# Optimization experiments

Measured on AMD Instinct MI355X. Metric: run time of the kernel, lower is better.

The kernel has to match this reference:

```python
import jax, jax.numpy as jnp
import numpy as np

NHEAD = 8
LAYER_NAMES = ('self', 'cross', 'self', 'cross')
EPS = 1e-6


def ln(x, g, b, eps=1e-5):
    m = jnp.mean(x, -1, keepdims=True)
    v = jnp.mean((x - m) ** 2, -1, keepdims=True)
    return (x - m) * jax.lax.rsqrt(v + eps) * g + b


def linear_attention(q, k, v, q_mask, kv_mask):
    # q: [N, L, H, D], k/v: [N, S, H, D]; LoFTR LinearAttention (elu+1 feature map)
    Q = jax.nn.elu(q) + 1.0
    K = jax.nn.elu(k) + 1.0
    if q_mask is not None:
        Q = Q * q_mask[:, :, None, None].astype(Q.dtype)
    if kv_mask is not None:
        mk = kv_mask[:, :, None, None].astype(K.dtype)
        K = K * mk
        v = v * mk
    v_len = v.shape[1]
    v = v / v_len
    KV = jnp.einsum('nshd,nshv->nhdv', K, v)
    Z = 1.0 / (jnp.einsum('nlhd,nhd->nlh', Q, K.sum(1)) + EPS)
    return jnp.einsum('nlhd,nhdv,nlh->nlhv', Q, KV, Z) * v_len


def enc_layer(x, src, q_mask, kv_mask, Wq, Wk, Wv, Wm, W1, W2, g1, b1, g2, b2):
    # x: [N, L, C], src: [N, S, C]
    N, L, C = x.shape
    S = src.shape[1]
    H, D = NHEAD, C // NHEAD
    q = (x @ Wq).reshape(N, L, H, D)
    k = (src @ Wk).reshape(N, S, H, D)
    v = (src @ Wv).reshape(N, S, H, D)
    msg = linear_attention(q, k, v, q_mask, kv_mask).reshape(N, L, C)
    msg = ln(msg @ Wm, g1, b1)
    msg = ln(jnp.tanh(jnp.concatenate([x, msg], axis=-1) @ W1) @ W2, g2, b2)
    return x + msg


def sample_descriptors(kp, fmap, s):
    # kp: [B, L, K, 2] (x, y) raw-image pixel coords; fmap: [B, C, H, W]; s: stride
    B, C, H, W = fmap.shape
    k = kp - s / 2 + 0.5
    denom = jnp.array([W * s - s / 2 - 0.5, H * s - s / 2 - 0.5], dtype=kp.dtype)
    k = (k / denom) * 2.0 - 1.0  # normalized [-1, 1]
    px = (k[..., 0] + 1.0) * 0.5 * (W - 1)  # align_corners=True grid_sample
    py = (k[..., 1] + 1.0) * 0.5 * (H - 1)
    x0 = jnp.floor(px)
    y0 = jnp.floor(py)
    wx = (px - x0)[..., None]
    wy = (py - y0)[..., None]
    x0i = jnp.clip(x0, 0, W - 1).astype(jnp.int32)
    x1i = jnp.clip(x0 + 1, 0, W - 1).astype(jnp.int32)
    y0i = jnp.clip(y0, 0, H - 1).astype(jnp.int32)
    y1i = jnp.clip(y0 + 1, 0, H - 1).astype(jnp.int32)
    fm = jnp.transpose(fmap, (0, 2, 3, 1))  # [B, H, W, C]
    bidx = jnp.arange(B)[:, None, None]
    g00 = fm[bidx, y0i, x0i]
    g01 = fm[bidx, y0i, x1i]
    g10 = fm[bidx, y1i, x0i]
    g11 = fm[bidx, y1i, x1i]
    out = (1 - wy) * ((1 - wx) * g00 + wx * g01) + wy * ((1 - wx) * g10 + wx * g11)
    # SuperPoint-style L2 normalization of sampled descriptors
    out = out / (jnp.linalg.norm(out, axis=-1, keepdims=True) + 1e-8)
    return out  # [B, L, K, C]


def geo_transformer(feat0, feat1, kp0_cross, kp1_cross, mask_self0, mask_self1,
                    mask_cross0, mask_cross1, Wq, Wk, Wv, Wm, W1, W2, g1, b1, g2, b2,
                    h0, w0, h1, w1, scale):
    B, L0, C = feat0.shape
    L1 = feat1.shape[1]
    K = kp0_cross.shape[2]
    for i, name in enumerate(LAYER_NAMES):
        p = (Wq[i], Wk[i], Wv[i], Wm[i], W1[i], W2[i], g1[i], b1[i], g2[i], b2[i])
        if name == 'self':
            # source = masked subset of x == full source with kv-mask (v_length cancels)
            feat0 = enc_layer(feat0, feat0, None, mask_self0, *p)
            feat1 = enc_layer(feat1, feat1, None, mask_self1, *p)
        else:
            fmap0 = jnp.transpose(feat0.reshape(B, h0, w0, C), (0, 3, 1, 2))
            fmap1 = jnp.transpose(feat1.reshape(B, h1, w1, C), (0, 3, 1, 2))
            f0c = sample_descriptors(kp0_cross, fmap0, scale)  # [B, L1, K, C]
            f1c = sample_descriptors(kp1_cross, fmap1, scale)  # [B, L0, K, C]
            x0 = feat0.reshape(B * L0, 1, C)
            x1 = feat1.reshape(B * L1, 1, C)
            nf0 = enc_layer(x0, f1c.reshape(B * L0, K, C), None,
                            mask_cross1.reshape(B * L0, K), *p)
            nf1 = enc_layer(x1, f0c.reshape(B * L1, K, C), None,
                            mask_cross0.reshape(B * L1, K), *p)
            feat0 = nf0.reshape(B, L0, C)
            feat1 = nf1.reshape(B, L1, C)
    return feat0, feat1


def setup_inputs() -> dict:
    key = jax.random.key(0)
    B, H0, W0, C, K, S, NL = 2, 64, 64, 256, 9, 8, 4
    L = H0 * W0
    ks = jax.random.split(key, 16)
    std = (2.0 / (C + C)) ** 0.5
    std2 = (2.0 / (2 * C + 2 * C)) ** 0.5
    std3 = (2.0 / (2 * C + C)) ** 0.5
    kp0 = jnp.stack([
        jax.random.uniform(ks[2], (B, L, K)) * (W0 * S),
        jax.random.uniform(ks[3], (B, L, K)) * (H0 * S)], axis=-1)
    kp1 = jnp.stack([
        jax.random.uniform(ks[4], (B, L, K)) * (W0 * S),
        jax.random.uniform(ks[5], (B, L, K)) * (H0 * S)], axis=-1)
    return {
        'feat0': jax.random.normal(ks[0], (B, L, C), jnp.float32),
        'feat1': jax.random.normal(ks[1], (B, L, C), jnp.float32),
        'kp0_cross': kp0.astype(jnp.float32),
        'kp1_cross': kp1.astype(jnp.float32),
        'mask_self0': jax.random.bernoulli(ks[6], 0.9, (B, L)),
        'mask_self1': jax.random.bernoulli(ks[7], 0.9, (B, L)),
        'mask_cross0': jax.random.bernoulli(ks[8], 0.8, (B, L, K)),
        'mask_cross1': jax.random.bernoulli(ks[9], 0.8, (B, L, K)),
        'Wq': jax.random.normal(ks[10], (NL, C, C), jnp.float32) * std,
        'Wk': jax.random.normal(ks[11], (NL, C, C), jnp.float32) * std,
        'Wv': jax.random.normal(ks[12], (NL, C, C), jnp.float32) * std,
        'Wm': jax.random.normal(ks[13], (NL, C, C), jnp.float32) * std,
        'W1': jax.random.normal(ks[14], (NL, 2 * C, 2 * C), jnp.float32) * std2,
        'W2': jax.random.normal(ks[15], (NL, 2 * C, C), jnp.float32) * std3,
        'g1': jnp.ones((NL, C), jnp.float32),
        'b1': jnp.zeros((NL, C), jnp.float32),
        'g2': jnp.ones((NL, C), jnp.float32),
        'b2': jnp.zeros((NL, C), jnp.float32),
        'h0': H0, 'w0': W0, 'h1': H0, 'w1': W0, 'scale': S,
    }


def reference(feat0, feat1, kp0_cross, kp1_cross, mask_self0, mask_self1,
              mask_cross0, mask_cross1, Wq, Wk, Wv, Wm, W1, W2, g1, b1, g2, b2,
              h0, w0, h1, w1, scale):
    return geo_transformer(feat0, feat1, kp0_cross, kp1_cross, mask_self0, mask_self1,
                           mask_cross0, mask_cross1, Wq, Wk, Wv, Wm, W1, W2,
                           g1, b1, g2, b2, h0, w0, h1, w1, scale)
```

## Files before the change

kernel.cpp:

```cpp
#include <hip/hip_runtime.h>
#include <cstddef>


#define NROWS 16384

typedef unsigned short ushort_t;
typedef __attribute__((ext_vector_type(8))) short short8;
typedef __attribute__((ext_vector_type(4))) float f32x4;
typedef __attribute__((ext_vector_type(4))) unsigned short ushort4_t;
typedef __attribute__((ext_vector_type(8))) unsigned short ushort8_t;

__device__ __forceinline__ float b2f(unsigned short u) {
    union { unsigned int i; float f; } v; v.i = (unsigned int)u << 16; return v.f;
}
__device__ __forceinline__ unsigned short f2b(float x) {
    union { float f; unsigned int i; } v; v.f = x;
    unsigned int r = v.i + 0x7fffu + ((v.i >> 16) & 1u);
    return (unsigned short)(r >> 16);
}
__device__ __forceinline__ float elu1(float x) {
    return x > 0.f ? x + 1.f : __expf(x);
}

#define ASYNC_COPY16(gptr, lptr) \
    __builtin_amdgcn_global_load_lds((const __attribute__((address_space(1))) void*)(gptr), \
                                     (__attribute__((address_space(3))) void*)(lptr), 16, 0, 0)

__global__ __launch_bounds__(256) void gemm_bf16_kernel(
    const ushort_t* __restrict__ A0, int lda0,
    const ushort_t* __restrict__ Wt, int ldw,
    ushort_t* __restrict__ C, int ldc, int Kd)
{
    __shared__ ushort_t As[128 * 64];
    __shared__ ushort_t Bs[128 * 64];

    int tid = threadIdx.x;
    int m0 = blockIdx.y * 128;
    int n0 = blockIdx.x * 128;
    int lane = tid & 63, w = tid >> 6;
    int wrow = w >> 1, wcol = w & 1;
    int quad = lane >> 4, l16 = lane & 15;

    f32x4 acc[4][4];
    #pragma unroll
    for (int i = 0; i < 4; i++)
        #pragma unroll
        for (int j = 0; j < 4; j++) acc[i][j] = (f32x4){0.f, 0.f, 0.f, 0.f};

    for (int kb = 0; kb < Kd; kb += 64) {
        #pragma unroll
        for (int q = 0; q < 4; q++) {
            int s = q * 256 + tid;
            int kk = s >> 9, p = s & 511;
            int row = p >> 2, c4 = p & 3;
            ASYNC_COPY16(A0 + (size_t)(m0 + row) * lda0 + kb + kk * 32 + c4 * 8,
                         (char*)As + s * 16);
        }
        #pragma unroll
        for (int q = 0; q < 4; q++) {
            int s = q * 256 + tid;
            int kk = s >> 9, p = s & 511;
            int row = p >> 2, c4 = p & 3;
            ASYNC_COPY16(Wt + (size_t)(n0 + row) * ldw + kb + kk * 32 + c4 * 8,
                         (char*)Bs + s * 16);
        }
        __syncthreads();

        #pragma unroll
        for (int kk = 0; kk < 2; kk++) {
            short8 af[4], bf[4];
            #pragma unroll
            for (int mt = 0; mt < 4; mt++)
                af[mt] = *(const short8*)&As[kk * 4096 + (wrow * 64 + mt * 16 + l16) * 32 + quad * 8];
            #pragma unroll
            for (int nt = 0; nt < 4; nt++)
                bf[nt] = *(const short8*)&Bs[kk * 4096 + (wcol * 64 + nt * 16 + l16) * 32 + quad * 8];
            #pragma unroll
            for (int mt = 0; mt < 4; mt++)
                #pragma unroll
                for (int nt = 0; nt < 4; nt++)
                    acc[mt][nt] = __builtin_amdgcn_mfma_f32_16x16x32_bf16(
                        af[mt], bf[nt], acc[mt][nt], 0, 0, 0);
        }
        __syncthreads();
    }

    #pragma unroll
    for (int mt = 0; mt < 4; mt++) {
        int row = m0 + wrow * 64 + mt * 16 + quad * 4;
        #pragma unroll
        for (int nt = 0; nt < 4; nt++) {
            int col = n0 + wcol * 64 + nt * 16 + l16;
            #pragma unroll
            for (int r = 0; r < 4; r++)
                C[(size_t)(row + r) * ldc + col] = f2b(acc[mt][nt][r]);
        }
    }
}

__global__ __launch_bounds__(256) void gemm_ln_kernel(
    const ushort_t* __restrict__ A, int lda,
    const ushort_t* __restrict__ Wt, int ldw, int Kd,
    const float* __restrict__ g, const float* __restrict__ bp,
    ushort_t* __restrict__ OutBf)
{
    __shared__ ushort_t As[32 * 64];
    __shared__ ushort_t Bs[256 * 64];
    __shared__ float rsum[4][32];
    __shared__ float rsq[4][32];

    int tid = threadIdx.x;
    int m0 = blockIdx.x * 32;
    int lane = tid & 63, w = tid >> 6;
    int quad = lane >> 4, l16 = lane & 15;

    f32x4 acc[2][4];
    #pragma unroll
    for (int i = 0; i < 2; i++)
        #pragma unroll
        for (int j = 0; j < 4; j++) acc[i][j] = (f32x4){0.f, 0.f, 0.f, 0.f};

    for (int kb = 0; kb < Kd; kb += 64) {
        {
            int s = tid;
            int kk = s >> 7, p = s & 127;
            int row = p >> 2, c4 = p & 3;
            ASYNC_COPY16(A + (size_t)(m0 + row) * lda + kb + kk * 32 + c4 * 8,
                         (char*)As + s * 16);
        }
        #pragma unroll
        for (int q = 0; q < 8; q++) {
            int s = q * 256 + tid;
            int kk = s >> 10, p = s & 1023;
            int row = p >> 2, c4 = p & 3;
            ASYNC_COPY16(Wt + (size_t)(row) * ldw + kb + kk * 32 + c4 * 8,
                         (char*)Bs + s * 16);
        }
        __syncthreads();

        #pragma unroll
        for (int kk = 0; kk < 2; kk++) {
            short8 af[2], bf[4];
            #pragma unroll
            for (int mt = 0; mt < 2; mt++)
                af[mt] = *(const short8*)&As[kk * 1024 + (mt * 16 + l16) * 32 + quad * 8];
            #pragma unroll
            for (int nt = 0; nt < 4; nt++)
                bf[nt] = *(const short8*)&Bs[kk * 8192 + (w * 64 + nt * 16 + l16) * 32 + quad * 8];
            #pragma unroll
            for (int mt = 0; mt < 2; mt++)
                #pragma unroll
                for (int nt = 0; nt < 4; nt++)
                    acc[mt][nt] = __builtin_amdgcn_mfma_f32_16x16x32_bf16(
                        af[mt], bf[nt], acc[mt][nt], 0, 0, 0);
        }
        __syncthreads();
    }

    #pragma unroll
    for (int mt = 0; mt < 2; mt++)
        #pragma unroll
        for (int r = 0; r < 4; r++) {
            float s = 0.f, q = 0.f;
            #pragma unroll
            for (int nt = 0; nt < 4; nt++) {
                float v = acc[mt][nt][r];
                s += v; q += v * v;
            }
            #pragma unroll
            for (int off = 1; off < 16; off <<= 1) {
                s += __shfl_xor(s, off, 64);
                q += __shfl_xor(q, off, 64);
            }
            if (l16 == 0) {
                rsum[w][mt * 16 + quad * 4 + r] = s;
                rsq[w][mt * 16 + quad * 4 + r]  = q;
            }
        }
    __syncthreads();

    #pragma unroll
    for (int mt = 0; mt < 2; mt++) {
        #pragma unroll
        for (int r = 0; r < 4; r++) {
            int rl = mt * 16 + quad * 4 + r;
            float s = rsum[0][rl] + rsum[1][rl] + rsum[2][rl] + rsum[3][rl];
            float q = rsq[0][rl] + rsq[1][rl] + rsq[2][rl] + rsq[3][rl];
            float m = s * (1.f / 256.f);
            float var = q * (1.f / 256.f) - m * m;
            float rs = rsqrtf(var + 1e-5f);
            size_t row = (size_t)(m0 + rl);
            #pragma unroll
            for (int nt = 0; nt < 4; nt++) {
                int col = w * 64 + nt * 16 + l16;
                float y = (acc[mt][nt][r] - m) * rs * g[col] + bp[col];
                OutBf[row * 256 + col] = f2b(y);
            }
        }
    }
}

__global__ __launch_bounds__(256) void mlp_fused_kernel(
    const ushort_t* __restrict__ Xb, const ushort_t* __restrict__ L1,
    const ushort_t* __restrict__ W1t, const ushort_t* __restrict__ W2t,
    const float* __restrict__ g, const float* __restrict__ bp,
    ushort_t* __restrict__ XbfOut, const float* __restrict__ Xin,
    float* __restrict__ Xout)
{
    __shared__ ushort_t Tt[32 * 512];
    __shared__ char buf[20480];

    ushort_t* As  = (ushort_t*)buf;
    ushort_t* Bs  = (ushort_t*)(buf + 4096);
    ushort_t* Bs2 = (ushort_t*)buf;
    float* rsum = (float*)buf;
    float* rsq  = (float*)(buf + 512);

    int tid = threadIdx.x;
    int m0 = blockIdx.x * 32;
    int lane = tid & 63, w = tid >> 6;
    int quad = lane >> 4, l16 = lane & 15;

    for (int np = 0; np < 4; np++) {
        f32x4 acc[2][2];
        #pragma unroll
        for (int i = 0; i < 2; i++)
            #pragma unroll
            for (int j = 0; j < 2; j++) acc[i][j] = (f32x4){0.f, 0.f, 0.f, 0.f};

        for (int kb = 0; kb < 512; kb += 64) {
            const ushort_t* Ab = (kb < 256) ? Xb : L1;
            int kc = (kb < 256) ? kb : kb - 256;
            {
                int s = tid;
                int kk = s >> 7, p = s & 127;
                ASYNC_COPY16(Ab + (size_t)(m0 + (p >> 2)) * 256 + kc + kk * 32 + (p & 3) * 8,
                             (char*)As + s * 16);
            }
            #pragma unroll
            for (int q = 0; q < 4; q++) {
                int s = q * 256 + tid;
                int kk = s >> 9, p = s & 511;
                ASYNC_COPY16(W1t + (size_t)(np * 128 + (p >> 2)) * 512 + kb + kk * 32 + (p & 3) * 8,
                             (char*)Bs + s * 16);
            }
            __syncthreads();

            #pragma unroll
            for (int kk = 0; kk < 2; kk++) {
                short8 af[2], bfr[2];
                #pragma unroll
                for (int mt = 0; mt < 2; mt++)
                    af[mt] = *(const short8*)&As[kk * 1024 + (mt * 16 + l16) * 32 + quad * 8];
                #pragma unroll
                for (int nt = 0; nt < 2; nt++)
                    bfr[nt] = *(const short8*)&Bs[kk * 4096 + (w * 32 + nt * 16 + l16) * 32 + quad * 8];
                #pragma unroll
                for (int mt = 0; mt < 2; mt++)
                    #pragma unroll
                    for (int nt = 0; nt < 2; nt++)
                        acc[mt][nt] = __builtin_amdgcn_mfma_f32_16x16x32_bf16(
                            af[mt], bfr[nt], acc[mt][nt], 0, 0, 0);
            }
            __syncthreads();
        }

        #pragma unroll
        for (int mt = 0; mt < 2; mt++)
            #pragma unroll
            for (int nt = 0; nt < 2; nt++)
                #pragma unroll
                for (int r = 0; r < 4; r++) {
                    int trow = mt * 16 + quad * 4 + r;
                    int col = np * 128 + w * 32 + nt * 16 + l16;
                    int c8s = (col >> 3) ^ (trow & 7);
                    Tt[trow * 512 + c8s * 8 + (col & 7)] = f2b(tanhf(acc[mt][nt][r]));
                }
    }

    f32x4 acc2[2][2][2];
    #pragma unroll
    for (int a = 0; a < 2; a++)
        #pragma unroll
        for (int i = 0; i < 2; i++)
            #pragma unroll
            for (int j = 0; j < 2; j++) acc2[a][i][j] = (f32x4){0.f, 0.f, 0.f, 0.f};

    for (int pass = 0; pass < 2; pass++) {
        for (int kb = 0; kb < 512; kb += 64) {
            #pragma unroll
            for (int q = 0; q < 4; q++) {
                int s = q * 256 + tid;
                int kk = s >> 9, p = s & 511;
                ASYNC_COPY16(W2t + (size_t)(pass * 128 + (p >> 2)) * 512 + kb + kk * 32 + (p & 3) * 8,
                             (char*)Bs2 + s * 16);
            }
            __syncthreads();

            #pragma unroll
            for (int kk = 0; kk < 2; kk++) {
                short8 af[2], bfr[2];
                #pragma unroll
                for (int mt = 0; mt < 2; mt++) {
                    int row = mt * 16 + l16;
                    int blk = ((kb >> 3) + kk * 4 + quad) ^ (row & 7);
                    af[mt] = *(const short8*)&Tt[row * 512 + blk * 8];
                }
                #pragma unroll
                for (int nt = 0; nt < 2; nt++)
                    bfr[nt] = *(const short8*)&Bs2[kk * 4096 + (w * 32 + nt * 16 + l16) * 32 + quad * 8];
                #pragma unroll
                for (int mt = 0; mt < 2; mt++)
                    #pragma unroll
                    for (int nt = 0; nt < 2; nt++)
                        acc2[pass][mt][nt] = __builtin_amdgcn_mfma_f32_16x16x32_bf16(
                            af[mt], bfr[nt], acc2[pass][mt][nt], 0, 0, 0);
            }
            __syncthreads();
        }
    }

    #pragma unroll
    for (int mt = 0; mt < 2; mt++)
        #pragma unroll
        for (int r = 0; r < 4; r++) {
            float s = 0.f, q = 0.f;
            #pragma unroll
            for (int pass = 0; pass < 2; pass++)
                #pragma unroll
                for (int nt = 0; nt < 2; nt++) {
                    float v = acc2[pass][mt][nt][r];
                    s += v; q += v * v;
                }
            #pragma unroll
            for (int off = 1; off < 16; off <<= 1) {
                s += __shfl_xor(s, off, 64);
                q += __shfl_xor(q, off, 64);
            }
            if (l16 == 0) {
                rsum[w * 32 + mt * 16 + quad * 4 + r] = s;
                rsq[w * 32 + mt * 16 + quad * 4 + r]  = q;
            }
        }
    __syncthreads();

    #pragma unroll
    for (int mt = 0; mt < 2; mt++) {
        #pragma unroll
        for (int r = 0; r < 4; r++) {
            int rl = mt * 16 + quad * 4 + r;
            float s = rsum[rl] + rsum[32 + rl] + rsum[64 + rl] + rsum[96 + rl];
            float q = rsq[rl] + rsq[32 + rl] + rsq[64 + rl] + rsq[96 + rl];
            float m = s * (1.f / 256.f);
            float var = q * (1.f / 256.f) - m * m;
            float rs = rsqrtf(var + 1e-5f);
            size_t row = (size_t)(m0 + rl);
            #pragma unroll
            for (int pass = 0; pass < 2; pass++)
                #pragma unroll
                for (int nt = 0; nt < 2; nt++) {
                    int col = pass * 128 + w * 32 + nt * 16 + l16;
                    float y = (acc2[pass][mt][nt][r] - m) * rs * g[col] + bp[col];
                    float xn = Xin[row * 256 + col] + y;
                    Xout[row * 256 + col] = xn;
                    XbfOut[row * 256 + col] = f2b(xn);
                }
        }
    }
}

__global__ __launch_bounds__(256) void wprep_kernel(
    const float* __restrict__ Wq, const float* __restrict__ Wk,
    const float* __restrict__ Wv, const float* __restrict__ Wm,
    const float* __restrict__ W1, const float* __restrict__ W2,
    ushort_t* __restrict__ Wqkvt, ushort_t* __restrict__ Wmt,
    ushort_t* __restrict__ W1t, ushort_t* __restrict__ W2t)
{
    int t = blockIdx.x;
    int layer = t / 640, r = t % 640;
    const float* src; ushort_t* dst;
    int ldsrc, lddst, tn, tk;
    if (r < 192) {
        int grp = r / 64, rr = r % 64; tn = rr / 8; tk = rr % 8;
        src = (grp == 0 ? Wq : grp == 1 ? Wk : Wv) + (size_t)layer * 65536;
        ldsrc = 256;
        dst = Wqkvt + (size_t)layer * 196608 + (size_t)grp * 65536;
        lddst = 256;
    } else if (r < 256) {
        int rr = r - 192; tn = rr / 8; tk = rr % 8;
        src = Wm + (size_t)layer * 65536; ldsrc = 256;
        dst = Wmt + (size_t)layer * 65536; lddst = 256;
    } else if (r < 512) {
        int rr = r - 256; tn = rr / 16; tk = rr % 16;
        src = W1 + (size_t)layer * 262144; ldsrc = 512;
        dst = W1t + (size_t)layer * 262144; lddst = 512;
    } else {
        int rr = r - 512; tn = rr / 16; tk = rr % 16;
        src = W2 + (size_t)layer * 131072; ldsrc = 256;
        dst = W2t + (size_t)layer * 131072; lddst = 512;
    }
    int n0 = tn * 32, k0 = tk * 32;
    __shared__ float tileS[32][33];
    int j = threadIdx.x & 31, i0 = threadIdx.x >> 5;
    #pragma unroll
    for (int p = 0; p < 4; p++) {
        int i = i0 + p * 8;
        tileS[i][j] = src[(size_t)(k0 + i) * ldsrc + n0 + j];
    }
    __syncthreads();
    #pragma unroll
    for (int p = 0; p < 4; p++) {
        int i = i0 + p * 8;
        dst[(size_t)(n0 + i) * lddst + k0 + j] = f2b(tileS[j][i]);
    }
}

__global__ __launch_bounds__(256) void init_kernel(
    const float* __restrict__ f0, const float* __restrict__ f1,
    float* __restrict__ X, ushort_t* __restrict__ Xbf)
{
    int idx = blockIdx.x * 256 + threadIdx.x;
    size_t e = (size_t)idx * 4;
    float4 v = (e < 2097152) ? *(const float4*)&f0[e] : *(const float4*)&f1[e - 2097152];
    *(float4*)&X[e] = v;
    ushort4_t u = { f2b(v.x), f2b(v.y), f2b(v.z), f2b(v.w) };
    *(ushort4_t*)&Xbf[e] = u;
}

__global__ __launch_bounds__(256) void kv_reduce_kernel(
    const ushort_t* __restrict__ QKV,
    const int* __restrict__ mask0, const int* __restrict__ mask1,
    float* __restrict__ KV, float* __restrict__ Ksum)
{
    int g = blockIdx.y;
    int t = g >> 4, b = (g >> 3) & 1, h = g & 7;
    const int* mask = t ? mask1 : mask0;
    int rowbase = t * 8192 + b * 4096;
    int s_begin = blockIdx.x * 256;

    __shared__ float sK[32][32];
    __shared__ float sV[32][32];

    int tid = threadIdx.x;
    int e  = tid & 31;
    int dq = tid >> 5;

    float acc[4] = {0.f, 0.f, 0.f, 0.f};
    float ks[4]  = {0.f, 0.f, 0.f, 0.f};

    for (int s0 = s_begin; s0 < s_begin + 256; s0 += 32) {
        #pragma unroll
        for (int q = 0; q < 2; q++) {
            int idx = tid + q * 256;
            int rl = idx >> 4;
            int part = idx & 15;
            int s = s0 + rl;
            size_t row = (size_t)(rowbase + s);
            float m = mask[b * 4096 + s] ? 1.f : 0.f;
            if (part < 8) {
                ushort4_t u = *(const ushort4_t*)&QKV[row * 768 + 256 + h * 32 + part * 4];
                float4 f = { elu1(b2f(u.x)) * m, elu1(b2f(u.y)) * m,
                             elu1(b2f(u.z)) * m, elu1(b2f(u.w)) * m };
                *(float4*)&sK[rl][part * 4] = f;
            } else {
                ushort4_t u = *(const ushort4_t*)&QKV[row * 768 + 512 + h * 32 + (part - 8) * 4];
                float4 f = { b2f(u.x) * m, b2f(u.y) * m, b2f(u.z) * m, b2f(u.w) * m };
                *(float4*)&sV[rl][(part - 8) * 4] = f;
            }
        }
        __syncthreads();

        #pragma unroll
        for (int s = 0; s < 32; s++) {
            float4 kq = *(const float4*)&sK[s][dq * 4];
            float vv = sV[s][e];
            acc[0] += kq.x * vv;
            acc[1] += kq.y * vv;
            acc[2] += kq.z * vv;
            acc[3] += kq.w * vv;
            ks[0] += kq.x; ks[1] += kq.y; ks[2] += kq.z; ks[3] += kq.w;
        }
        __syncthreads();
    }

    #pragma unroll
    for (int j = 0; j < 4; j++)
        atomicAdd(&KV[(size_t)g * 1024 + (dq * 4 + j) * 32 + e], acc[j]);
    if (e == 0) {
        #pragma unroll
        for (int j = 0; j < 4; j++)
            atomicAdd(&Ksum[g * 32 + dq * 4 + j], ks[j]);
    }
}

__global__ __launch_bounds__(256) void attn_apply_kernel(
    const ushort_t* __restrict__ QKV, const float* __restrict__ KV,
    const float* __restrict__ Ksum, ushort_t* __restrict__ MSG)
{
    int row = blockIdx.x;
    int t = row >> 13, bb = (row >> 12) & 1;
    int gb = (t * 2 + bb) * 8;
    int c = threadIdx.x, h = c >> 5, e = c & 31;
    int g = gb + h;

    __shared__ float sQ[256];
    float qf = elu1(b2f(QKV[(size_t)row * 768 + c]));
    sQ[c] = qf;
    __syncthreads();

    float p = qf * Ksum[g * 32 + e];
    #pragma unroll
    for (int off = 16; off; off >>= 1) p += __shfl_xor(p, off, 32);
    float Z = 1.f / (p + 1e-6f);

    float acc = 0.f;
    #pragma unroll
    for (int d = 0; d < 32; d++)
        acc += sQ[h * 32 + d] * KV[(size_t)g * 1024 + d * 32 + e];

    MSG[(size_t)row * 256 + c] = f2b(acc * Z);
}

__global__ __launch_bounds__(256) void gram_kernel(
    const ushort_t* __restrict__ Xbf, float* __restrict__ Gm)
{
    int a = blockIdx.x * 4 + (threadIdx.x >> 6);
    int lane = threadIdx.x & 63;
    int img = a / 4225;
    int rr = a - img * 4225;
    int ay = rr / 65, ax = rr - ay * 65;
    int xa = ax > 0 ? ax - 1 : 0;
    int xb = ax < 64 ? ax : 63;
    if (ax == 0) xb = 0;
    int ya = ay > 0 ? ay - 1 : 0;
    int yb = ay < 64 ? ay : 63;
    if (ay == 0) yb = 0;

    size_t rbase = (size_t)img * 4096;
    size_t r0 = (rbase + ya * 64 + xa) * 256;
    size_t r1 = (rbase + ya * 64 + xb) * 256;
    size_t r2 = (rbase + yb * 64 + xa) * 256;
    size_t r3 = (rbase + yb * 64 + xb) * 256;

    int c4 = lane * 4;
    ushort4_t u0 = *(const ushort4_t*)&Xbf[r0 + c4];
    ushort4_t u1 = *(const ushort4_t*)&Xbf[r1 + c4];
    ushort4_t u2 = *(const ushort4_t*)&Xbf[r2 + c4];
    ushort4_t u3 = *(const ushort4_t*)&Xbf[r3 + c4];

    float p[10] = {0,0,0,0,0,0,0,0,0,0};
    #pragma unroll
    for (int j = 0; j < 4; j++) {
        float f0 = b2f(u0[j]), f1 = b2f(u1[j]), f2 = b2f(u2[j]), f3 = b2f(u3[j]);
        p[0] += f0 * f0; p[1] += f0 * f1; p[2] += f0 * f2; p[3] += f0 * f3;
        p[4] += f1 * f1; p[5] += f1 * f2; p[6] += f1 * f3;
        p[7] += f2 * f2; p[8] += f2 * f3; p[9] += f3 * f3;
    }
    #pragma unroll
    for (int k = 0; k < 10; k++)
        #pragma unroll
        for (int off = 32; off; off >>= 1) p[k] += __shfl_xor(p[k], off, 64);

    if (lane == 0) {
        #pragma unroll
        for (int k = 0; k < 10; k++) Gm[(size_t)a * 10 + k] = p[k];
    }
}

__global__ __launch_bounds__(256) void cross_fused_kernel(
    const ushort_t* __restrict__ QKV, const float* __restrict__ Gm,
    const float* __restrict__ kp0, const float* __restrict__ kp1,
    const int* __restrict__ maskc0, const int* __restrict__ maskc1,
    ushort_t* __restrict__ MSG)
{
    int wv = threadIdx.x >> 6;
    int lane = threadIdx.x & 63;
    int half = lane >> 5;
    int l32 = lane & 31;
    int row = blockIdx.x * 4 + wv;

    int t = row >> 13;
    int bl = row & 8191;
    int ts = 1 - t;
    const float* kp = ts ? kp1 : kp0;
    const int* mask = (t == 0) ? maskc1 : maskc0;
    int img = ts * 2 + (bl >> 12);
    size_t rb = (size_t)img * 4096;
    const float* Gimg = Gm + (size_t)img * 42250;

    int c8 = l32 * 8;

    ushort8_t qu = *(const ushort8_t*)&QKV[(size_t)row * 768 + c8];
    float qf[8];
    #pragma unroll
    for (int j = 0; j < 8; j++) qf[j] = elu1(b2f(qu[j]));

    float zsum = 0.f;
    float acc[8] = {0,0,0,0,0,0,0,0};

    for (int s9 = half; s9 < 9; s9 += 2) {
        int r = bl * 9 + s9;
        bool mk = mask[r] != 0;
        if (mk) {
            float xx = kp[(size_t)r * 2 + 0];
            float yy = kp[(size_t)r * 2 + 1];
            float px = (xx - 3.5f) * (63.f / 507.5f);
            float py = (yy - 3.5f) * (63.f / 507.5f);
            float fx = floorf(px), fy = floorf(py);
            float wx = px - fx, wy = py - fy;
            int ix = (int)fx, iy = (int)fy;
            int xa = ix > 0 ? ix : 0;
            int xb = ix + 1 > 0 ? (ix + 1 < 63 ? ix + 1 : 63) : 0;
            int ya = iy > 0 ? iy : 0;
            int yb = iy + 1 > 0 ? (iy + 1 < 63 ? iy + 1 : 63) : 0;

            float w0 = (1.f - wy) * (1.f - wx);
            float w1 = (1.f - wy) * wx;
            float w2 = wy * (1.f - wx);
            float w3 = wy * wx;

            const float* G = &Gimg[(size_t)((iy + 1) * 65 + (ix + 1)) * 10];
            float g00 = G[0], g01 = G[1], g02 = G[2], g03 = G[3], g11 = G[4];
            float g12 = G[5], g13 = G[6], g22 = G[7], g23 = G[8], g33 = G[9];
            float ss = w0 * w0 * g00 + w1 * w1 * g11 + w2 * w2 * g22 + w3 * w3 * g33
                     + 2.f * (w0 * w1 * g01 + w0 * w2 * g02 + w0 * w3 * g03
                            + w1 * w2 * g12 + w1 * w3 * g13 + w2 * w3 * g23);
            float inv = 1.f / (sqrtf(ss) + 1e-8f);
            float u0 = w0 * inv, u1 = w1 * inv, u2 = w2 * inv, u3 = w3 * inv;

            size_t s00 = (rb + ya * 64 + xa) * 768;
            size_t s01 = (rb + ya * 64 + xb) * 768;
            size_t s10 = (rb + yb * 64 + xa) * 768;
            size_t s11 = (rb + yb * 64 + xb) * 768;

            ushort8_t k00 = *(const ushort8_t*)&QKV[s00 + 256 + c8];
            ushort8_t k01 = *(const ushort8_t*)&QKV[s01 + 256 + c8];
            ushort8_t k10 = *(const ushort8_t*)&QKV[s10 + 256 + c8];
            ushort8_t k11 = *(const ushort8_t*)&QKV[s11 + 256 + c8];
            ushort8_t v00 = *(const ushort8_t*)&QKV[s00 + 512 + c8];
            ushort8_t v01 = *(const ushort8_t*)&QKV[s01 + 512 + c8];
            ushort8_t v10 = *(const ushort8_t*)&QKV[s10 + 512 + c8];
            ushort8_t v11 = *(const ushort8_t*)&QKV[s11 + 512 + c8];

            float vc[8];
            float p = 0.f;
            #pragma unroll
            for (int j = 0; j < 8; j++) {
                float kc = u0 * b2f(k00[j]) + u1 * b2f(k01[j])
                         + u2 * b2f(k10[j]) + u3 * b2f(k11[j]);
                vc[j] = u0 * b2f(v00[j]) + u1 * b2f(v01[j])
                      + u2 * b2f(v10[j]) + u3 * b2f(v11[j]);
                p += qf[j] * elu1(kc);
            }
            p += __shfl_xor(p, 1, 64);
            p += __shfl_xor(p, 2, 64);

            zsum += p;
            #pragma unroll
            for (int j = 0; j < 8; j++) acc[j] += p * vc[j];
        }
    }

    zsum += __shfl_xor(zsum, 32, 64);
    #pragma unroll
    for (int j = 0; j < 8; j++) acc[j] += __shfl_xor(acc[j], 32, 64);

    if (half == 0) {
        float Z = 1.f / (zsum + 1e-6f);
        ushort8_t o;
        #pragma unroll
        for (int j = 0; j < 8; j++) o[j] = f2b(acc[j] * Z);
        *(ushort8_t*)&MSG[(size_t)row * 256 + c8] = o;
    }
}


extern "C" void kernel_launch(void* const* d_in, const int* in_sizes, int n_in,
                              void* d_out, int out_size, void* d_ws, size_t ws_size,
                              hipStream_t stream)
{
    const float* feat0 = (const float*)d_in[0];
    const float* feat1 = (const float*)d_in[1];
    const float* kp0 = (const float*)d_in[2];
    const float* kp1 = (const float*)d_in[3];
    const int* ms0 = (const int*)d_in[4];
    const int* ms1 = (const int*)d_in[5];
    const int* mc0 = (const int*)d_in[6];
    const int* mc1 = (const int*)d_in[7];
    const float* Wq = (const float*)d_in[8];
    const float* Wk = (const float*)d_in[9];
    const float* Wv = (const float*)d_in[10];
    const float* Wm = (const float*)d_in[11];
    const float* W1 = (const float*)d_in[12];
    const float* W2 = (const float*)d_in[13];
    const float* g1 = (const float*)d_in[14];
    const float* b1 = (const float*)d_in[15];
    const float* g2 = (const float*)d_in[16];
    const float* b2 = (const float*)d_in[17];

    char* p = (char*)d_ws;
    float*    X     = (float*)p;            p += 16777216;
    ushort_t* Xbf   = (ushort_t*)p;         p += 8388608;
    ushort_t* QKV   = (ushort_t*)p;         p += 25165824;
    ushort_t* MSG   = (ushort_t*)p;         p += 8388608;
    ushort_t* L1bf  = (ushort_t*)p;         p += 8388608;
    float*    KVb   = (float*)p;            p += 131072;
    float*    KSb   = (float*)p;            p += 4096;
    float*    Gm    = (float*)p;            p += 679936;
    ushort_t* Wqkvt = (ushort_t*)p;         p += 1572864;
    ushort_t* Wmt   = (ushort_t*)p;         p += 524288;
    ushort_t* W1t   = (ushort_t*)p;         p += 2097152;
    ushort_t* W2t   = (ushort_t*)p;         p += 1048576;

    init_kernel<<<4096, 256, 0, stream>>>(feat0, feat1, X, Xbf);
    wprep_kernel<<<2560, 256, 0, stream>>>(Wq, Wk, Wv, Wm, W1, W2, Wqkvt, Wmt, W1t, W2t);

    for (int i = 0; i < 4; i++) {
        const ushort_t* Wqkvt_l = Wqkvt + (size_t)i * 196608;
        const ushort_t* Wmt_l   = Wmt   + (size_t)i * 65536;
        const ushort_t* W1t_l   = W1t   + (size_t)i * 262144;
        const ushort_t* W2t_l   = W2t   + (size_t)i * 131072;
        const float* g1_l = g1 + (size_t)i * 256;
        const float* b1_l = b1 + (size_t)i * 256;
        const float* g2_l = g2 + (size_t)i * 256;
        const float* b2_l = b2 + (size_t)i * 256;
        bool is_self = (i == 0 || i == 2);

        gemm_bf16_kernel<<<dim3(6, 128), 256, 0, stream>>>(
            Xbf, 256, Wqkvt_l, 256, QKV, 768, 256);

        if (is_self) {
            hipMemsetAsync(KVb, 0, 33792 * 4, stream);
            kv_reduce_kernel<<<dim3(16, 32), 256, 0, stream>>>(QKV, ms0, ms1, KVb, KSb);
            attn_apply_kernel<<<NROWS, 256, 0, stream>>>(QKV, KVb, KSb, MSG);
        } else {
            gram_kernel<<<4225, 256, 0, stream>>>(Xbf, Gm);
            cross_fused_kernel<<<NROWS / 4, 256, 0, stream>>>(QKV, Gm, kp0, kp1, mc0, mc1, MSG);
        }

        gemm_ln_kernel<<<NROWS / 32, 256, 0, stream>>>(
            MSG, 256, Wmt_l, 256, 256, g1_l, b1_l, L1bf);

        float* Xout = (i == 3) ? (float*)d_out : X;
        mlp_fused_kernel<<<NROWS / 32, 256, 0, stream>>>(
            Xbf, L1bf, W1t_l, W2t_l, g2_l, b2_l, Xbf, X, Xout);
    }
}
```

Baseline: 613.4 us.

## Fold KV zeroing into QKV GEMM and batch cross-attention gathers

The hipMemsetAsync that cleared the KV accumulator is removed, and the first row of blocks of the QKV GEMM zeroes that buffer instead, saving one launch per self layer. The Gram buffer stride is padded from 10 to 12 floats so each entry can be read with vectorised float4/float2 loads. The cross-attention kernel is split into two phases: first it computes all sample weights and offsets, then it issues the gathers. It also gets a 4-blocks-per-SM launch bound, so the independent memory loads can overlap. The costs are higher register pressure, a slightly larger Gram buffer, and a reliance on stream ordering so the zeroing finishes before kv_reduce runs.

```diff
diff --git a/kernel.cpp b/kernel.cpp
--- a/kernel.cpp
+++ b/kernel.cpp
@@ -29,7 +29,8 @@
 __global__ __launch_bounds__(256) void gemm_bf16_kernel(
     const ushort_t* __restrict__ A0, int lda0,
     const ushort_t* __restrict__ Wt, int ldw,
-    ushort_t* __restrict__ C, int ldc, int Kd)
+    ushort_t* __restrict__ C, int ldc, int Kd,
+    float* __restrict__ zbuf, int znf4)
 {
     __shared__ ushort_t As[128 * 64];
     __shared__ ushort_t Bs[128 * 64];
@@ -40,6 +41,12 @@
     int lane = tid & 63, w = tid >> 6;
     int wrow = w >> 1, wcol = w & 1;
     int quad = lane >> 4, l16 = lane & 15;
+
+    if (zbuf && blockIdx.y == 0) {
+        int nblk = gridDim.x;
+        for (int i = blockIdx.x * 256 + tid; i < znf4; i += nblk * 256)
+            *(float4*)&zbuf[(size_t)i * 4] = (float4){0.f, 0.f, 0.f, 0.f};
+    }
 
     f32x4 acc[4][4];
     #pragma unroll
@@ -563,11 +570,11 @@
 
     if (lane == 0) {
         #pragma unroll
-        for (int k = 0; k < 10; k++) Gm[(size_t)a * 10 + k] = p[k];
-    }
-}
-
-__global__ __launch_bounds__(256) void cross_fused_kernel(
+        for (int k = 0; k < 10; k++) Gm[(size_t)a * 12 + k] = p[k];
+    }
+}
+
+__global__ __launch_bounds__(256, 4) void cross_fused_kernel(
     const ushort_t* __restrict__ QKV, const float* __restrict__ Gm,
     const float* __restrict__ kp0, const float* __restrict__ kp1,
     const int* __restrict__ maskc0, const int* __restrict__ maskc1,
@@ -586,7 +593,7 @@
     const int* mask = (t == 0) ? maskc1 : maskc0;
     int img = ts * 2 + (bl >> 12);
     size_t rb = (size_t)img * 4096;
-    const float* Gimg = Gm + (size_t)img * 42250;
+    const float* Gimg = Gm + (size_t)img * 50700;
 
     int c8 = l32 * 8;
 
@@ -595,17 +602,19 @@
     #pragma unroll
     for (int j = 0; j < 8; j++) qf[j] = elu1(b2f(qu[j]));
 
-    float zsum = 0.f;
-    float acc[8] = {0,0,0,0,0,0,0,0};
-
-    for (int s9 = half; s9 < 9; s9 += 2) {
-        int r = bl * 9 + s9;
-        bool mk = mask[r] != 0;
+    int oA[5], oB[5];
+    float u0a[5], u1a[5], u2a[5], u3a[5];
+    int mbits = 0;
+    #pragma unroll
+    for (int i = 0; i < 5; i++) {
+        int s9 = 2 * i + half;
+        bool valid = s9 < 9;
+        int r = bl * 9 + (valid ? s9 : 0);
+        bool mk = valid && (mask[r] != 0);
         if (mk) {
-            float xx = kp[(size_t)r * 2 + 0];
-            float yy = kp[(size_t)r * 2 + 1];
-            float px = (xx - 3.5f) * (63.f / 507.5f);
-            float py = (yy - 3.5f) * (63.f / 507.5f);
+            float2 kxy = *(const float2*)&kp[(size_t)r * 2];
+            float px = (kxy.x - 3.5f) * (63.f / 507.5f);
+            float py = (kxy.y - 3.5f) * (63.f / 507.5f);
             float fx = floorf(px), fy = floorf(py);
             float wx = px - fx, wy = py - fy;
             int ix = (int)fx, iy = (int)fy;
@@ -619,19 +628,31 @@
             float w2 = wy * (1.f - wx);
             float w3 = wy * wx;
 
-            const float* G = &Gimg[(size_t)((iy + 1) * 65 + (ix + 1)) * 10];
-            float g00 = G[0], g01 = G[1], g02 = G[2], g03 = G[3], g11 = G[4];
-            float g12 = G[5], g13 = G[6], g22 = G[7], g23 = G[8], g33 = G[9];
-            float ss = w0 * w0 * g00 + w1 * w1 * g11 + w2 * w2 * g22 + w3 * w3 * g33
-                     + 2.f * (w0 * w1 * g01 + w0 * w2 * g02 + w0 * w3 * g03
-                            + w1 * w2 * g12 + w1 * w3 * g13 + w2 * w3 * g23);
+            const float* G = &Gimg[(size_t)((iy + 1) * 65 + (ix + 1)) * 12];
+            float4 ga = *(const float4*)&G[0];
+            float4 gb4 = *(const float4*)&G[4];
+            float2 gc = *(const float2*)&G[8];
+            float ss = w0 * w0 * ga.x + w1 * w1 * gb4.x + w2 * w2 * gb4.w + w3 * w3 * gc.y
+                     + 2.f * (w0 * w1 * ga.y + w0 * w2 * ga.z + w0 * w3 * ga.w
+                            + w1 * w2 * gb4.y + w1 * w3 * gb4.z + w2 * w3 * gc.x);
             float inv = 1.f / (sqrtf(ss) + 1e-8f);
-            float u0 = w0 * inv, u1 = w1 * inv, u2 = w2 * inv, u3 = w3 * inv;
-
-            size_t s00 = (rb + ya * 64 + xa) * 768;
-            size_t s01 = (rb + ya * 64 + xb) * 768;
-            size_t s10 = (rb + yb * 64 + xa) * 768;
-            size_t s11 = (rb + yb * 64 + xb) * 768;
+            u0a[i] = w0 * inv; u1a[i] = w1 * inv; u2a[i] = w2 * inv; u3a[i] = w3 * inv;
+            oA[i] = (ya * 64 + xa) | ((ya * 64 + xb) << 16);
+            oB[i] = (yb * 64 + xa) | ((yb * 64 + xb) << 16);
+            mbits |= 1 << i;
+        }
+    }
+
+    float zsum = 0.f;
+    float acc[8] = {0,0,0,0,0,0,0,0};
+    #pragma unroll
+    for (int i = 0; i < 5; i++) {
+        if ((mbits >> i) & 1) {
+            size_t s00 = (rb + (oA[i] & 0xffff)) * 768;
+            size_t s01 = (rb + (oA[i] >> 16)) * 768;
+            size_t s10 = (rb + (oB[i] & 0xffff)) * 768;
+            size_t s11 = (rb + (oB[i] >> 16)) * 768;
+            float u0 = u0a[i], u1 = u1a[i], u2 = u2a[i], u3 = u3a[i];
 
             ushort8_t k00 = *(const ushort8_t*)&QKV[s00 + 256 + c8];
             ushort8_t k01 = *(const ushort8_t*)&QKV[s01 + 256 + c8];
@@ -706,7 +727,7 @@
     ushort_t* L1bf  = (ushort_t*)p;         p += 8388608;
     float*    KVb   = (float*)p;            p += 131072;
     float*    KSb   = (float*)p;            p += 4096;
-    float*    Gm    = (float*)p;            p += 679936;
+    float*    Gm    = (float*)p;            p += 811264;
     ushort_t* Wqkvt = (ushort_t*)p;         p += 1572864;
     ushort_t* Wmt   = (ushort_t*)p;         p += 524288;
     ushort_t* W1t   = (ushort_t*)p;         p += 2097152;
@@ -727,10 +748,10 @@
         bool is_self = (i == 0 || i == 2);
 
         gemm_bf16_kernel<<<dim3(6, 128), 256, 0, stream>>>(
-            Xbf, 256, Wqkvt_l, 256, QKV, 768, 256);
+            Xbf, 256, Wqkvt_l, 256, QKV, 768, 256,
+            is_self ? KVb : nullptr, 33792 / 4);
 
         if (is_self) {
-            hipMemsetAsync(KVb, 0, 33792 * 4, stream);
             kv_reduce_kernel<<<dim3(16, 32), 256, 0, stream>>>(QKV, ms0, ms1, KVb, KSb);
             attn_apply_kernel<<<NROWS, 256, 0, stream>>>(QKV, KVb, KSb, MSG);
         } else {
```

Measured after the change: 631.2 us. +2.9%, slower.
